# Optimization experiments

Measured on AMD Instinct MI355X. Metric: run time of the kernel, lower is better.

The kernel has to match this reference:

```python
import jax, jax.numpy as jnp
import numpy as np

B, S, IN = 64, 2048, 256          # batch, num_steps, input_size
MS, H, HD = 8, 8, 64              # mem_slots, num_heads, head_size
M = H * HD                        # mem_size = 512
KS = HD                           # key_size defaults to head_size
NG = 2 * M                        # num_gates (gate_style='unit')
TOPK = 3
EPS = 1e-5


def layernorm(x, g, b):
    mu = jnp.mean(x, axis=-1, keepdims=True)
    var = jnp.var(x, axis=-1, keepdims=True)
    return (x - mu) / jnp.sqrt(var + EPS) * g + b


def setup_inputs() -> dict:
    key = jax.random.key(0)
    ks = jax.random.split(key, 16)
    def w(k, shape, scale=0.02):
        return jax.random.normal(k, shape, dtype=jnp.float32) * scale
    return {
        "inputs": jax.random.normal(ks[0], (B, S, IN), dtype=jnp.float32),
        "memory": jax.random.normal(ks[1], (B, MS, M), dtype=jnp.float32),
        "Wq": w(ks[2], (M, H * KS)), "bq": jnp.zeros((H * KS,), jnp.float32),
        "Wk": w(ks[3], (M, H * KS)), "bk": jnp.zeros((H * KS,), jnp.float32),
        "Wv": w(ks[4], (M, H * HD)), "bv": jnp.zeros((H * HD,), jnp.float32),
        "Wmlp": w(ks[5], (M, M)), "bmlp": jnp.zeros((M,), jnp.float32),  # shared across both mlp layers ([Linear]*L)
        "g1": jnp.ones((M,), jnp.float32), "b1": jnp.zeros((M,), jnp.float32),
        "g2": jnp.ones((M,), jnp.float32), "b2": jnp.zeros((M,), jnp.float32),
        "Wi": w(ks[6], (IN, M)), "bi": jnp.zeros((M,), jnp.float32),  # input_projector
        "rw": jax.random.normal(ks[7], (M,), dtype=jnp.float32),       # RepeatLinear.w
        "Wr": w(ks[8], (M, NG)), "br": jnp.zeros((NG,), jnp.float32),  # RepeatLinear.linear
        "Wg": w(ks[9], (MS, M, NG)),                                   # GroupLinearLayer (no bias)
        "forget_bias": jnp.array(1.0, jnp.float32),
        "input_bias": jnp.array(0.0, jnp.float32),
    }


def reference(inputs, memory, Wq, bq, Wk, bk, Wv, bv, Wmlp, bmlp,
              g1, b1, g2, b2, Wi, bi, rw, Wr, br, Wg,
              forget_bias, input_bias):
    # input_projector (treat_input_as_matrix=True path)
    x = inputs @ Wi + bi                                   # [B,S,M]

    # --- multihead attention over memory (num_blocks=1) ---
    q = (memory @ Wq + bq).reshape(B, MS, H, KS).transpose(0, 2, 1, 3)   # [B,H,MS,KS]
    k = (x @ Wk + bk).reshape(B, S, H, KS).transpose(0, 2, 1, 3)         # [B,H,S,KS]
    v = (x @ Wv + bv).reshape(B, S, H, HD).transpose(0, 2, 1, 3)         # [B,H,S,HD]
    scores = jax.nn.softmax(jnp.einsum('bhmd,bhsd->bhms', q, k), axis=-1)  # no 1/sqrt(d) scale, per source
    # top-k mask over key/step axis, scatter of top-k indices -> multiplicative 0/1 mask
    _, idx = jax.lax.top_k(scores, TOPK)                   # [B,H,MS,TOPK]
    mask = jnp.sum(jax.nn.one_hot(idx, S, dtype=scores.dtype), axis=-2)  # [B,H,MS,S]
    scores = scores * mask
    att = jnp.einsum('bhms,bhsd->bhmd', scores, v)         # [B,H,MS,HD]
    att = att.transpose(0, 2, 1, 3).reshape(B, MS, M)      # [B,MS,M]

    mem1 = layernorm(memory + att, g1, b1)
    mlp = jax.nn.relu(mem1 @ Wmlp + bmlp)                  # attention_mlp layer (weights shared)
    mlp = jax.nn.relu(mlp @ Wmlp + bmlp)
    next_mem = layernorm(mem1 + mlp, g2, b2)

    # --- gates (computed from pre-attention memory, per forward_step) ---
    gate_in = jax.nn.relu(rw * x).mean(axis=1) @ Wr + br   # RepeatLinear -> [B,NG]
    gate_mem = jnp.einsum('bsd,sdo->bso', jnp.tanh(memory), Wg)  # GroupLinear -> [B,MS,NG]
    gates = gate_mem + gate_in[:, None, :]
    input_gate, forget_gate = jnp.split(gates, 2, axis=2)  # each [B,MS,M]
    input_gate = jax.nn.sigmoid(input_gate + input_bias)
    forget_gate = jax.nn.sigmoid(forget_gate + forget_bias)

    next_mem = input_gate * jnp.tanh(next_mem) + forget_gate * memory
    return next_mem.reshape(B, MS * M)
```

## Files before the change

### kernel.cpp

```cpp
#include <hip/hip_runtime.h>
#include <hip/hip_bf16.h>
#include <math.h>

#define BB 64
#define SS 2048
#define IN_ 256
#define MSLOT 8
#define HH 8
#define HD_ 64
#define MM 512
#define NG_ 1024

typedef __attribute__((ext_vector_type(8))) short short8;
typedef __attribute__((ext_vector_type(8))) unsigned short ushort8;
typedef __attribute__((ext_vector_type(4))) unsigned short ushort4v;
typedef __attribute__((ext_vector_type(4))) float f32x4;
typedef __attribute__((ext_vector_type(16))) float f32x16;
typedef unsigned long long u64;
typedef unsigned int u32;

__device__ __forceinline__ unsigned short f2bf(float f) {
    unsigned int u = __builtin_bit_cast(unsigned int, f);
    u += 0x7fff + ((u >> 16) & 1);
    return (unsigned short)(u >> 16);
}

__device__ __forceinline__ u32 f2bf_pk(float a, float b) {
    u32 r;
    asm("v_cvt_pk_bf16_f32 %0, %1, %2" : "=v"(r) : "v"(a), "v"(b));
    return r;
}

__device__ __forceinline__ u64 score_key(float v, int idx) {
    u32 x = __float_as_uint(v);
    u32 fk = (x & 0x80000000u) ? ~x : (x | 0x80000000u);
    return ((u64)fk << 32) | (u32)(~(u32)idx);
}
__device__ __forceinline__ float key_val(u64 k) {
    u32 fk = (u32)(k >> 32);
    u32 x = (fk & 0x80000000u) ? (fk & 0x7FFFFFFFu) : ~fk;
    return __uint_as_float(x);
}
__device__ __forceinline__ int key_idx(u64 k) { return (int)(~(u32)k); }

__device__ __forceinline__ void merge3(u64& a0, u64& a1, u64& a2, u64 b0, u64 b1, u64 b2) {
    bool t0 = a0 >= b0;
    u64 m0 = t0 ? a0 : b0;
    u64 a0x = t0 ? a1 : a0, a1x = t0 ? a2 : a1;
    u64 b0x = t0 ? b0 : b1, b1x = t0 ? b1 : b2;
    bool t1 = a0x >= b0x;
    u64 m1 = t1 ? a0x : b0x;
    u64 a0y = t1 ? a1x : a0x;
    u64 b0y = t1 ? b0x : b1x;
    bool t2 = a0y >= b0y;
    u64 m2 = t2 ? a0y : b0y;
    a0 = m0; a1 = m1; a2 = m2;
}

__device__ __forceinline__ void merge3_shfl(u64& k0, u64& k1, u64& k2, int off) {
    u64 b0 = __shfl_xor(k0, off);
    u64 b1 = __shfl_xor(k1, off);
    u64 b2 = __shfl_xor(k2, off);
    merge3(k0, k1, k2, b0, b1, b2);
}

__device__ __forceinline__ float block_sum256(float v, float* red) {
    int t = threadIdx.x;
    red[t] = v; __syncthreads();
    for (int s = 128; s > 0; s >>= 1) {
        if (t < s) red[t] += red[t + s];
        __syncthreads();
    }
    float r = red[0];
    __syncthreads();
    return r;
}

__device__ __forceinline__ void stage_tile_f32cvt(unsigned short* lds,
                                                  const float* __restrict__ src,
                                                  int t) {
#pragma unroll
    for (int it = 0; it < 8; ++it) {
        int c = t + it * 256;
        int r = c >> 5, ch = c & 31;
        const float* p = src + (size_t)r * 256 + ch * 8;
        float4 f0 = *(const float4*)p;
        float4 f1 = *(const float4*)(p + 4);
        uint4 v;
        v.x = f2bf_pk(f0.x, f0.y);
        v.y = f2bf_pk(f0.z, f0.w);
        v.z = f2bf_pk(f1.x, f1.y);
        v.w = f2bf_pk(f1.z, f1.w);
        int sch = ch ^ (r & 15);
        *(uint4*)(lds + r * 256 + sch * 8) = v;
    }
}

__device__ __forceinline__ short8 frag_ld(const unsigned short* lds, int row, int chunk) {
    int sch = chunk ^ (row & 15);
    return *(const short8*)(lds + row * 256 + sch * 8);
}

__device__ __forceinline__ short8 frag_ld512(const unsigned short* lds, int row, int chunk) {
    int sch = chunk ^ (row & 7);
    return *(const short8*)(lds + row * 512 + sch * 8);
}

__global__ __launch_bounds__(256) void k_fuse_w2(const float* __restrict__ Wi,
                                                 const float* __restrict__ Wk,
                                                 const float* __restrict__ Wv,
                                                 const float* __restrict__ bi,
                                                 const float* __restrict__ bv,
                                                 float* __restrict__ WikT,
                                                 float* __restrict__ Wiv,
                                                 float* __restrict__ bvf) {
    int blk = blockIdx.x;
    int t = threadIdx.x;
    if (blk >= 256) {
        int o = (blk - 256) * 256 + t;
        float acc = bv[o];
        for (int j = 0; j < 512; ++j) acc += bi[j] * Wv[j * 512 + o];
        bvf[o] = acc;
        return;
    }
    int which = blk >> 7;
    int rem = blk & 127;
    int ot = rem >> 3, it = rem & 7;
    int o0 = ot * 32, i0 = it * 32;
    const float* W = which ? Wv : Wk;

    __shared__ float As[64 * 33];
    __shared__ float Bs[32 * 65];
    int tx = t & 15, ty = t >> 4;

    float acc[2][2] = {{0.f, 0.f}, {0.f, 0.f}};
    for (int jc = 0; jc < 512; jc += 64) {
        __syncthreads();
#pragma unroll
        for (int k = 0; k < 8; ++k) {
            int idx = t + k * 256;
            int jl = idx >> 5, ol = idx & 31;
            As[jl * 33 + ol] = W[(jc + jl) * 512 + o0 + ol];
        }
#pragma unroll
        for (int k = 0; k < 8; ++k) {
            int idx = t + k * 256;
            int il = idx >> 6, jl = idx & 63;
            Bs[il * 65 + jl] = Wi[(i0 + il) * 512 + jc + jl];
        }
        __syncthreads();
#pragma unroll 4
        for (int jl = 0; jl < 64; ++jl) {
            float a0 = As[jl * 33 + ty], a1 = As[jl * 33 + ty + 16];
            float b0 = Bs[tx * 65 + jl], b1 = Bs[(tx + 16) * 65 + jl];
            acc[0][0] += a0 * b0; acc[0][1] += a0 * b1;
            acc[1][0] += a1 * b0; acc[1][1] += a1 * b1;
        }
    }
#pragma unroll
    for (int m = 0; m < 2; ++m)
#pragma unroll
        for (int n = 0; n < 2; ++n) {
            int o = o0 + ty + 16 * m, i = i0 + tx + 16 * n;
            if (which) Wiv[i * 512 + o] = acc[m][n];
            else       WikT[o * 256 + i] = acc[m][n];
        }
}

__global__ __launch_bounds__(256) void k_q2(const float* __restrict__ memory,
                                            const float* __restrict__ Wq,
                                            const float* __restrict__ bq,
                                            float* __restrict__ q) {
    int blk = blockIdx.x;
    int bt = blk >> 4, ot2 = blk & 15;
    int b0 = bt * 32, o0 = ot2 * 32;
    int t = threadIdx.x;
    __shared__ float Am[32 * 65];
    __shared__ float Bq[64 * 33];
    int tx = t & 15, ty = t >> 4;
    float acc[2][2] = {{0.f, 0.f}, {0.f, 0.f}};
    for (int jc = 0; jc < 512; jc += 64) {
        __syncthreads();
#pragma unroll
        for (int k = 0; k < 8; ++k) {
            int idx = t + k * 256;
            int bl = idx >> 6, jl = idx & 63;
            Am[bl * 65 + jl] = memory[(b0 + bl) * 512 + jc + jl];
        }
#pragma unroll
        for (int k = 0; k < 8; ++k) {
            int idx = t + k * 256;
            int jl = idx >> 5, ol = idx & 31;
            Bq[jl * 33 + ol] = Wq[(jc + jl) * 512 + o0 + ol];
        }
        __syncthreads();
#pragma unroll 4
        for (int jl = 0; jl < 64; ++jl) {
            float a0 = Am[ty * 65 + jl], a1 = Am[(ty + 16) * 65 + jl];
            float b0v = Bq[jl * 33 + tx], b1v = Bq[jl * 33 + tx + 16];
            acc[0][0] += a0 * b0v; acc[0][1] += a0 * b1v;
            acc[1][0] += a1 * b0v; acc[1][1] += a1 * b1v;
        }
    }
#pragma unroll
    for (int m = 0; m < 2; ++m)
#pragma unroll
        for (int n = 0; n < 2; ++n) {
            int bms = b0 + ty + 16 * m, o = o0 + tx + 16 * n;
            q[bms * 512 + o] = acc[m][n] + bq[o];
        }
}

__global__ __launch_bounds__(256) void k_p(const float* __restrict__ q,
                                           const float* __restrict__ WikT,
                                           unsigned short* __restrict__ Pb) {
    int blk = blockIdx.x;
    int b = blk >> 6, hm = blk & 63;
    int h = hm >> 3, ms = hm & 7;
    int t = threadIdx.x;
    __shared__ float qv[64];
    if (t < 64) qv[t] = q[(b * 8 + ms) * 512 + h * 64 + t];
    __syncthreads();
    float acc = 0.f;
    for (int d = 0; d < 64; ++d) acc += qv[d] * WikT[(h * 64 + d) * 256 + t];
    Pb[blk * 256 + t] = f2bf(acc);
}

__global__ __launch_bounds__(256) void k_prep(const float* __restrict__ Wi,
                                              unsigned short* __restrict__ WiTf,
                                              const float* __restrict__ mem,
                                              unsigned short* __restrict__ tm,
                                              const float* __restrict__ Wmlp,
                                              unsigned short* __restrict__ WmlpTb) {
    int blk = blockIdx.x;
    int t = threadIdx.x;
    if (blk < 512) {
        int idx = blk * 256 + t;
        int e = idx & 7, l = (idx >> 3) & 63, ks = (idx >> 9) & 15, dtg = idx >> 13;
        int d = dtg * 32 + (l & 31);
        int k = ks * 16 + (l >> 5) * 8 + e;
        WiTf[idx] = f2bf(Wi[k * 512 + d]);
    } else if (blk < 768) {
        int i = ((blk - 512) * 256 + t) * 4;
        float4 v = *(const float4*)(mem + i);
        ushort4v o;
        o[0] = f2bf(tanhf(v.x)); o[1] = f2bf(tanhf(v.y));
        o[2] = f2bf(tanhf(v.z)); o[3] = f2bf(tanhf(v.w));
        *(ushort4v*)(tm + i) = o;
    } else {
        int o = blk - 768;
#pragma unroll
        for (int kk = 0; kk < 2; ++kk) {
            int k = kk * 256 + t;
            WmlpTb[o * 512 + k] = f2bf(Wmlp[k * 512 + o]);
        }
    }
}

__global__ __launch_bounds__(256) void k_big(const float* __restrict__ inputs,
                                             const unsigned short* __restrict__ Pb,
                                             const unsigned short* __restrict__ WiTf,
                                             const float* __restrict__ bi,
                                             const float* __restrict__ rw,
                                             uint4* __restrict__ statA,
                                             uint4* __restrict__ statB,
                                             float* __restrict__ giaccp) {
    __shared__ unsigned short Il[64 * 256];
    int t = threadIdx.x;
    int hw = blockIdx.x;
    int L = (hw & 7) * 256 + (hw >> 3);
    int b = L >> 5, stile = L & 31;
    int l = t & 63, w = t >> 6;
    int kg = l >> 4, r16 = l & 15;
    int l31 = l & 31, hi = l >> 5;

    short8 a[8];
    {
        const unsigned short* pbase = Pb + ((size_t)(b * 64 + w * 16 + r16)) * 256;
#pragma unroll
        for (int kk = 0; kk < 8; ++kk)
            a[kk] = *(const short8*)(pbase + kk * 32 + kg * 8);
    }

    stage_tile_f32cvt(Il, inputs + ((size_t)b * SS + stile * 64) * IN_, t);
    __syncthreads();

    f32x4 acc[4];
#pragma unroll
    for (int nt = 0; nt < 4; ++nt) acc[nt] = (f32x4){0.f, 0.f, 0.f, 0.f};
#pragma unroll
    for (int kk = 0; kk < 8; ++kk) {
#pragma unroll
        for (int nt = 0; nt < 4; ++nt) {
            short8 bfr = frag_ld(Il, nt * 16 + r16, kk * 4 + kg);
            acc[nt] = __builtin_amdgcn_mfma_f32_16x16x32_bf16(a[kk], bfr, acc[nt], 0, 0, 0);
        }
    }

#pragma unroll 1
    for (int i = 0; i < 4; ++i) {
        int dtg = w * 4 + i;
        int d = dtg * 32 + l31;
        float bid = bi[d], rwd = rw[d];
        f32x16 g0 = {0.f,0.f,0.f,0.f,0.f,0.f,0.f,0.f,0.f,0.f,0.f,0.f,0.f,0.f,0.f,0.f};
        f32x16 g1 = {0.f,0.f,0.f,0.f,0.f,0.f,0.f,0.f,0.f,0.f,0.f,0.f,0.f,0.f,0.f,0.f};
#pragma unroll
        for (int ksh = 0; ksh < 2; ++ksh) {
            short8 wf[8];
#pragma unroll
            for (int ks8 = 0; ks8 < 8; ++ks8)
                wf[ks8] = *(const short8*)(WiTf + ((size_t)((dtg * 16 + ksh * 8 + ks8) * 64) + l) * 8);
#pragma unroll
            for (int ks8 = 0; ks8 < 8; ++ks8) {
                int ch = (ksh * 8 + ks8) * 2 + hi;
                short8 a0 = frag_ld(Il, l31, ch);
                g0 = __builtin_amdgcn_mfma_f32_32x32x16_bf16(a0, wf[ks8], g0, 0, 0, 0);
                short8 a1 = frag_ld(Il, 32 + l31, ch);
                g1 = __builtin_amdgcn_mfma_f32_32x32x16_bf16(a1, wf[ks8], g1, 0, 0, 0);
            }
        }
        float rs = 0.f;
#pragma unroll
        for (int jj = 0; jj < 16; ++jj) {
            rs += fmaxf(rwd * (g0[jj] + bid), 0.f);
            rs += fmaxf(rwd * (g1[jj] + bid), 0.f);
        }
        rs += __shfl_xor(rs, 32);
        if (hi == 0)
            giaccp[((size_t)stile * 64 + b) * 512 + d] = rs;
    }

    __syncthreads();
    float* Sl = (float*)Il;
#pragma unroll
    for (int nt = 0; nt < 4; ++nt)
#pragma unroll
        for (int j = 0; j < 4; ++j)
            Sl[(w * 16 + kg * 4 + j) * 65 + nt * 16 + r16] = acc[nt][j];
    __syncthreads();

    int row = t >> 2, cq = t & 3;
    float v[16];
#pragma unroll
    for (int i = 0; i < 16; ++i) v[i] = Sl[row * 65 + cq * 16 + i];

    u64 k0 = 0, k1 = 0, k2 = 0;
#pragma unroll
    for (int i = 0; i < 16; ++i) {
        u64 key = score_key(v[i], stile * 64 + cq * 16 + i);
        bool g0 = key > k0, g1 = key > k1, g2 = key > k2;
        k2 = g1 ? k1 : (g2 ? key : k2);
        k1 = g0 ? k0 : (g1 ? key : k1);
        k0 = g0 ? key : k0;
    }
    merge3_shfl(k0, k1, k2, 1);
    merge3_shfl(k0, k1, k2, 2);

    float m = key_val(k0);
    float se = 0.f;
#pragma unroll
    for (int i = 0; i < 16; ++i) se += expf(v[i] - m);
    se += __shfl_xor(se, 1);
    se += __shfl_xor(se, 2);

    if (cq == 0) {
        int grow = (b * 64 + row) * 32 + stile;
        statA[grow] = make_uint4(__float_as_uint(se), (u32)(k0 >> 32), (u32)k0, (u32)(k1 >> 32));
        statB[grow] = make_uint4((u32)k1, (u32)(k2 >> 32), (u32)k2, 0u);
    }
}

__global__ __launch_bounds__(256) void k_combine(const uint4* __restrict__ statA,
                                                 const uint4* __restrict__ statB,
                                                 float* __restrict__ topk_p,
                                                 int* __restrict__ topk_idx) {
    int t = threadIdx.x;
    int row = blockIdx.x * 4 + (t >> 6);
    int l = t & 63;

    float s_c = 0.f, m_c = 0.f;
    u64 k0 = 0, k1 = 0, k2 = 0;
    if (l < 32) {
        uint4 A = statA[row * 32 + l];
        uint4 Bv = statB[row * 32 + l];
        s_c = __uint_as_float(A.x);
        k0 = ((u64)A.y << 32) | A.z;
        k1 = ((u64)A.w << 32) | Bv.x;
        k2 = ((u64)Bv.y << 32) | Bv.z;
        m_c = key_val(k0);
    }
    merge3_shfl(k0, k1, k2, 1);
    merge3_shfl(k0, k1, k2, 2);
    merge3_shfl(k0, k1, k2, 4);
    merge3_shfl(k0, k1, k2, 8);
    merge3_shfl(k0, k1, k2, 16);

    float M = key_val(k0);
    float S = (l < 32) ? s_c * expf(m_c - M) : 0.f;
#pragma unroll
    for (int off = 1; off <= 16; off <<= 1) S += __shfl_xor(S, off);

    if (l == 0) {
        u64 ks[3] = {k0, k1, k2};
#pragma unroll
        for (int r = 0; r < 3; ++r) {
            topk_p[row * 3 + r] = expf(key_val(ks[r]) - M) / S;
            topk_idx[row * 3 + r] = key_idx(ks[r]);
        }
    }
}

__global__ __launch_bounds__(256) void k_att2(const float* __restrict__ inputs,
                                              const float* __restrict__ Wiv,
                                              const float* __restrict__ bvf,
                                              const float* __restrict__ topk_p,
                                              const int* __restrict__ topk_idx,
                                              const float* __restrict__ memory,
                                              const float* __restrict__ g1,
                                              const float* __restrict__ b1,
                                              float* __restrict__ mem1) {
    int bms = blockIdx.x;
    int b = bms >> 3, ms = bms & 7;
    int t = threadIdx.x;
    __shared__ float w[8 * 256];
    __shared__ float ps[8];
    __shared__ float red[256];

#pragma unroll
    for (int h = 0; h < 8; ++h) {
        int row = (b * 64 + h * 8 + ms) * 3;
        float acc = 0.f, psum = 0.f;
#pragma unroll
        for (int j = 0; j < 3; ++j) {
            int sj = topk_idx[row + j];
            float pj = topk_p[row + j];
            acc += pj * inputs[((size_t)b * SS + sj) * IN_ + t];
            psum += pj;
        }
        w[h * 256 + t] = acc;
        if (t == 0) ps[h] = psum;
    }
    __syncthreads();

    float a_val[2];
#pragma unroll
    for (int oo = 0; oo < 2; ++oo) {
        int o = oo * 256 + t;
        int h = o >> 6;
        float acc = ps[h] * bvf[o];
        const float* wh = w + h * 256;
#pragma unroll 8
        for (int i = 0; i < 256; ++i) acc += wh[i] * Wiv[i * 512 + o];
        a_val[oo] = acc;
    }

    float m0 = memory[bms * 512 + t], m1 = memory[bms * 512 + t + 256];
    float x0 = m0 + a_val[0], x1 = m1 + a_val[1];
    float mu = block_sum256(x0 + x1, red) * (1.f / 512.f);
    float d0 = x0 - mu, d1 = x1 - mu;
    float var = block_sum256(d0 * d0 + d1 * d1, red) * (1.f / 512.f);
    float rstd = rsqrtf(var + 1e-5f);
    mem1[bms * 512 + t]       = d0 * rstd * g1[t] + b1[t];
    mem1[bms * 512 + t + 256] = d1 * rstd * g1[t + 256] + b1[t + 256];
}

__global__ __launch_bounds__(256) void k_gatein2(const float* __restrict__ giaccp,
                                                 const float* __restrict__ Wr,
                                                 const float* __restrict__ br,
                                                 float* __restrict__ gate_in) {
    int b = blockIdx.x >> 2, ot = blockIdx.x & 3;
    int t = threadIdx.x;
    int o = ot * 256 + t;
    __shared__ float gm[512];
    float s0 = 0.f, s1 = 0.f;
    for (int st = 0; st < 32; ++st) {
        s0 += giaccp[((size_t)st * 64 + b) * 512 + t];
        s1 += giaccp[((size_t)st * 64 + b) * 512 + t + 256];
    }
    gm[t]       = s0 * (1.0f / 2048.0f);
    gm[t + 256] = s1 * (1.0f / 2048.0f);
    __syncthreads();
    float acc = br[o];
#pragma unroll 8
    for (int d = 0; d < 512; ++d) acc += gm[d] * Wr[d * 1024 + o];
    gate_in[b * 1024 + o] = acc;
}

__global__ __launch_bounds__(256) void k_gates_mfma(const unsigned short* __restrict__ tmem_b,
                                                    const float* __restrict__ Wg,
                                                    const float* __restrict__ gate_in,
                                                    const float* __restrict__ fb,
                                                    const float* __restrict__ ib,
                                                    float* __restrict__ sg) {
    int ms = blockIdx.x >> 5;
    int otile = blockIdx.x & 31;
    int t = threadIdx.x;
    int l = t & 63, w = t >> 6;
    int kg = l >> 4, r16 = l & 15;
    __shared__ unsigned short Al[64 * 128];
    __shared__ unsigned short Bl[32 * 136];
    f32x4 acc[2];
#pragma unroll
    for (int nt = 0; nt < 2; ++nt) acc[nt] = (f32x4){0.f, 0.f, 0.f, 0.f};

    int o_l = t & 31;
    for (int kc = 0; kc < 4; ++kc) {
        __syncthreads();
#pragma unroll
        for (int it = 0; it < 4; ++it) {
            int c = t + it * 256;
            int r = c >> 4, ch = c & 15;
            ushort8 v = *(const ushort8*)(tmem_b + (size_t)(r * 8 + ms) * 512 + kc * 128 + ch * 8);
            int sch = ch ^ (r & 7);
            *(ushort8*)(Al + r * 128 + sch * 8) = v;
        }
#pragma unroll
        for (int i = 0; i < 16; ++i) {
            int k_l = (t >> 5) + 8 * i;
            float v = Wg[((size_t)ms * 512 + kc * 128 + k_l) * 1024 + otile * 32 + o_l];
            Bl[o_l * 136 + k_l] = f2bf(v);
        }
        __syncthreads();
#pragma unroll
        for (int kk = 0; kk < 4; ++kk) {
            int ch = kk * 4 + kg;
            short8 a = *(const short8*)(Al + (w * 16 + r16) * 128 + ((ch ^ (r16 & 7)) * 8));
#pragma unroll
            for (int nt = 0; nt < 2; ++nt) {
                short8 bfr = *(const short8*)(Bl + (nt * 16 + r16) * 136 + ch * 8);
                acc[nt] = __builtin_amdgcn_mfma_f32_16x16x32_bf16(a, bfr, acc[nt], 0, 0, 0);
            }
        }
    }
    float ibv = ib[0], fbv = fb[0];
#pragma unroll
    for (int nt = 0; nt < 2; ++nt) {
        int o = otile * 32 + nt * 16 + r16;
        float bias = (o < 512) ? ibv : fbv;
#pragma unroll
        for (int j = 0; j < 4; ++j) {
            int b = w * 16 + kg * 4 + j;
            float g = acc[nt][j] + gate_in[b * 1024 + o] + bias;
            sg[(size_t)(b * 8 + ms) * 1024 + o] = 1.f / (1.f + expf(-g));
        }
    }
}

__global__ __launch_bounds__(256) void k_mlp_mfma(const float* __restrict__ mem1,
                                                  const unsigned short* __restrict__ WmlpTb,
                                                  const float* __restrict__ bmlp,
                                                  const float* __restrict__ g2,
                                                  const float* __restrict__ b2,
                                                  const float* __restrict__ sg,
                                                  const float* __restrict__ memory,
                                                  float* __restrict__ out) {
    __shared__ unsigned short At[16 * 512];
    __shared__ unsigned short Bt[16 * 512];
    __shared__ float redS[64], redQ[64], muL[16], rsL[16];
    int blk = blockIdx.x;
    int rowbase = blk * 16;
    int t = threadIdx.x;
    int l = t & 63, w = t >> 6;
    int kg = l >> 4, r16 = l & 15;

#pragma unroll
    for (int it = 0; it < 4; ++it) {
        int c = t + it * 256;
        int r = c >> 6, ch = c & 63;
        const float* p = mem1 + (size_t)(rowbase + r) * 512 + ch * 8;
        float4 f0 = *(const float4*)p;
        float4 f1 = *(const float4*)(p + 4);
        uint4 v;
        v.x = f2bf_pk(f0.x, f0.y);
        v.y = f2bf_pk(f0.z, f0.w);
        v.z = f2bf_pk(f1.x, f1.y);
        v.w = f2bf_pk(f1.z, f1.w);
        int sch = ch ^ (r & 7);
        *(uint4*)(At + r * 512 + sch * 8) = v;
    }
    __syncthreads();

    f32x4 acc[8];
#pragma unroll
    for (int f = 0; f < 8; ++f) acc[f] = (f32x4){0.f, 0.f, 0.f, 0.f};
    for (int kk2 = 0; kk2 < 16; ++kk2) {
        short8 a = frag_ld512(At, r16, kk2 * 4 + kg);
#pragma unroll
        for (int f = 0; f < 8; ++f) {
            short8 bfr = *(const short8*)(WmlpTb + (size_t)(w * 128 + f * 16 + r16) * 512 + kk2 * 32 + kg * 8);
            acc[f] = __builtin_amdgcn_mfma_f32_16x16x32_bf16(a, bfr, acc[f], 0, 0, 0);
        }
    }
#pragma unroll
    for (int f = 0; f < 8; ++f) {
        int o = w * 128 + f * 16 + r16;
        float bm = bmlp[o];
        int ch = o >> 3, oe = o & 7;
#pragma unroll
        for (int j = 0; j < 4; ++j) {
            int row = kg * 4 + j;
            float v = fmaxf(acc[f][j] + bm, 0.f);
            Bt[row * 512 + ((ch ^ (row & 7)) * 8 + oe)] = f2bf(v);
        }
    }
    __syncthreads();

#pragma unroll
    for (int f = 0; f < 8; ++f) acc[f] = (f32x4){0.f, 0.f, 0.f, 0.f};
    for (int kk2 = 0; kk2 < 16; ++kk2) {
        short8 a = frag_ld512(Bt, r16, kk2 * 4 + kg);
#pragma unroll
        for (int f = 0; f < 8; ++f) {
            short8 bfr = *(const short8*)(WmlpTb + (size_t)(w * 128 + f * 16 + r16) * 512 + kk2 * 32 + kg * 8);
            acc[f] = __builtin_amdgcn_mfma_f32_16x16x32_bf16(a, bfr, acc[f], 0, 0, 0);
        }
    }

    float y[8][4];
    float ps[4] = {0.f, 0.f, 0.f, 0.f}, pq[4] = {0.f, 0.f, 0.f, 0.f};
#pragma unroll
    for (int f = 0; f < 8; ++f) {
        int o = w * 128 + f * 16 + r16;
        float bm = bmlp[o];
#pragma unroll
        for (int j = 0; j < 4; ++j) {
            int row = kg * 4 + j;
            float m1v = mem1[(size_t)(rowbase + row) * 512 + o];
            float v = m1v + fmaxf(acc[f][j] + bm, 0.f);
            y[f][j] = v;
            ps[j] += v;
            pq[j] += v * v;
        }
    }
#pragma unroll
    for (int j = 0; j < 4; ++j) {
#pragma unroll
        for (int off = 1; off <= 8; off <<= 1) {
            ps[j] += __shfl_xor(ps[j], off);
            pq[j] += __shfl_xor(pq[j], off);
        }
    }
    if (r16 == 0) {
#pragma unroll
        for (int j = 0; j < 4; ++j) {
            int row = kg * 4 + j;
            redS[row * 4 + w] = ps[j];
            redQ[row * 4 + w] = pq[j];
        }
    }
    __syncthreads();
    if (t < 16) {
        float s = redS[t * 4] + redS[t * 4 + 1] + redS[t * 4 + 2] + redS[t * 4 + 3];
        float q = redQ[t * 4] + redQ[t * 4 + 1] + redQ[t * 4 + 2] + redQ[t * 4 + 3];
        float mu = s * (1.f / 512.f);
        float var = q * (1.f / 512.f) - mu * mu;
        muL[t] = mu;
        rsL[t] = rsqrtf(var + 1e-5f);
    }
    __syncthreads();

#pragma unroll
    for (int f = 0; f < 8; ++f) {
        int o = w * 128 + f * 16 + r16;
        float g2v = g2[o], b2v = b2[o];
#pragma unroll
        for (int j = 0; j < 4; ++j) {
            int row = kg * 4 + j;
            int grow = rowbase + row;
            float np = (y[f][j] - muL[row]) * rsL[row] * g2v + b2v;
            float ig = sg[(size_t)grow * 1024 + o];
            float fg = sg[(size_t)grow * 1024 + 512 + o];
            float mv = memory[(size_t)grow * 512 + o];
            out[(size_t)grow * 512 + o] = ig * tanhf(np) + fg * mv;
        }
    }
}

extern "C" void kernel_launch(void* const* d_in, const int* in_sizes, int n_in,
                              void* d_out, int out_size, void* d_ws, size_t ws_size,
                              hipStream_t stream) {
    const float* inputs = (const float*)d_in[0];
    const float* memory = (const float*)d_in[1];
    const float* Wq  = (const float*)d_in[2];
    const float* bq  = (const float*)d_in[3];
    const float* Wk  = (const float*)d_in[4];
    const float* Wv  = (const float*)d_in[6];
    const float* bv  = (const float*)d_in[7];
    const float* Wmlp= (const float*)d_in[8];
    const float* bmlp= (const float*)d_in[9];
    const float* g1  = (const float*)d_in[10];
    const float* b1  = (const float*)d_in[11];
    const float* g2  = (const float*)d_in[12];
    const float* b2  = (const float*)d_in[13];
    const float* Wi  = (const float*)d_in[14];
    const float* bi  = (const float*)d_in[15];
    const float* rw  = (const float*)d_in[16];
    const float* Wr  = (const float*)d_in[17];
    const float* br  = (const float*)d_in[18];
    const float* Wg  = (const float*)d_in[19];
    const float* fb  = (const float*)d_in[20];
    const float* ib  = (const float*)d_in[21];
    float* out = (float*)d_out;

    float* ws = (float*)d_ws;
    float* WikT   = ws + 0;
    float* Wiv    = ws + 131072;
    float* bvf    = ws + 262144;
    float* qbuf   = ws + 263168;
    unsigned short* Pb   = (unsigned short*)(ws + 525312);
    unsigned short* WiTf = (unsigned short*)(ws + 1049600);
    uint4* statA  = (uint4*)(ws + 1115136);
    uint4* statB  = (uint4*)(ws + 1639424);
    float* topkp  = ws + 2163712;
    int*   topki  = (int*)(ws + 2176000);
    float* giaccp = ws + 2188288;
    float* gatein = ws + 3236864;
    float* sgbuf  = ws + 3302400;
    float* mem1   = ws + 3826688;
    unsigned short* tmem_b = (unsigned short*)(ws + 4088832);
    unsigned short* WmlpTb = (unsigned short*)(ws + 4219904);

    (void)in_sizes; (void)n_in; (void)out_size; (void)ws_size;

    k_fuse_w2<<<258, 256, 0, stream>>>(Wi, Wk, Wv, bi, bv, WikT, Wiv, bvf);
    k_q2<<<256, 256, 0, stream>>>(memory, Wq, bq, qbuf);
    k_p<<<4096, 256, 0, stream>>>(qbuf, WikT, Pb);
    k_prep<<<1280, 256, 0, stream>>>(Wi, WiTf, memory, tmem_b, Wmlp, WmlpTb);
    k_big<<<2048, 256, 0, stream>>>(inputs, Pb, WiTf, bi, rw, statA, statB, giaccp);
    k_combine<<<1024, 256, 0, stream>>>(statA, statB, topkp, topki);
    k_gatein2<<<256, 256, 0, stream>>>(giaccp, Wr, br, gatein);
    k_gates_mfma<<<256, 256, 0, stream>>>(tmem_b, Wg, gatein, fb, ib, sgbuf);
    k_att2<<<512, 256, 0, stream>>>(inputs, Wiv, bvf, topkp, topki, memory, g1, b1, mem1);
    k_mlp_mfma<<<32, 256, 0, stream>>>(mem1, WmlpTb, bmlp, g2, b2, sgbuf, memory, out);
}
```

Measured before the change: 300.5 us.

## Merge small kernels into fewer launches and restructure k_big MFMA tiling

Folds k_fuse_w2, k_q2 and k_prep into one k_pre launch, merges k_combine with k_gatein2 into k_mid, and merges k_gates_mfma with k_att2 into k_post. This removes launch gaps and tail idling between small dependent kernels. k_big now computes scores with 32x32x16 MFMAs and a separate LDS score buffer, and splits the input-projection work across waves by sequence half and d-group. Partial gate sums double in count (giaccp layout grows), so workspace offsets shift. The extra LDS could lower occupancy in k_big.

```diff
diff --git a/kernel.cpp b/kernel.cpp
--- a/kernel.cpp
+++ b/kernel.cpp
@@ -106,109 +106,131 @@
     return *(const short8*)(lds + row * 512 + sch * 8);
 }
 
-__global__ __launch_bounds__(256) void k_fuse_w2(const float* __restrict__ Wi,
-                                                 const float* __restrict__ Wk,
-                                                 const float* __restrict__ Wv,
-                                                 const float* __restrict__ bi,
-                                                 const float* __restrict__ bv,
-                                                 float* __restrict__ WikT,
-                                                 float* __restrict__ Wiv,
-                                                 float* __restrict__ bvf) {
+__global__ __launch_bounds__(256) void k_pre(const float* __restrict__ Wi,
+                                             const float* __restrict__ Wk,
+                                             const float* __restrict__ Wv,
+                                             const float* __restrict__ bi,
+                                             const float* __restrict__ bv,
+                                             const float* __restrict__ memory,
+                                             const float* __restrict__ Wq,
+                                             const float* __restrict__ bq,
+                                             const float* __restrict__ Wmlp,
+                                             float* __restrict__ WikT,
+                                             float* __restrict__ Wiv,
+                                             float* __restrict__ bvf,
+                                             float* __restrict__ q,
+                                             unsigned short* __restrict__ WiTf,
+                                             unsigned short* __restrict__ tm,
+                                             unsigned short* __restrict__ WmlpTb) {
+    __shared__ float As[64 * 33];
+    __shared__ float Bs[32 * 65];
     int blk = blockIdx.x;
     int t = threadIdx.x;
-    if (blk >= 256) {
+
+    if (blk < 256) {
+        int which = blk >> 7;
+        int rem = blk & 127;
+        int ot = rem >> 3, it = rem & 7;
+        int o0 = ot * 32, i0 = it * 32;
+        const float* W = which ? Wv : Wk;
+        int tx = t & 15, ty = t >> 4;
+        float acc[2][2] = {{0.f, 0.f}, {0.f, 0.f}};
+        for (int jc = 0; jc < 512; jc += 64) {
+            __syncthreads();
+#pragma unroll
+            for (int k = 0; k < 8; ++k) {
+                int idx = t + k * 256;
+                int jl = idx >> 5, ol = idx & 31;
+                As[jl * 33 + ol] = W[(jc + jl) * 512 + o0 + ol];
+            }
+#pragma unroll
+            for (int k = 0; k < 8; ++k) {
+                int idx = t + k * 256;
+                int il = idx >> 6, jl = idx & 63;
+                Bs[il * 65 + jl] = Wi[(i0 + il) * 512 + jc + jl];
+            }
+            __syncthreads();
+#pragma unroll 4
+            for (int jl = 0; jl < 64; ++jl) {
+                float a0 = As[jl * 33 + ty], a1 = As[jl * 33 + ty + 16];
+                float b0 = Bs[tx * 65 + jl], b1 = Bs[(tx + 16) * 65 + jl];
+                acc[0][0] += a0 * b0; acc[0][1] += a0 * b1;
+                acc[1][0] += a1 * b0; acc[1][1] += a1 * b1;
+            }
+        }
+#pragma unroll
+        for (int m = 0; m < 2; ++m)
+#pragma unroll
+            for (int n = 0; n < 2; ++n) {
+                int o = o0 + ty + 16 * m, i = i0 + tx + 16 * n;
+                if (which) Wiv[i * 512 + o] = acc[m][n];
+                else       WikT[o * 256 + i] = acc[m][n];
+            }
+    } else if (blk < 258) {
         int o = (blk - 256) * 256 + t;
         float acc = bv[o];
         for (int j = 0; j < 512; ++j) acc += bi[j] * Wv[j * 512 + o];
         bvf[o] = acc;
-        return;
-    }
-    int which = blk >> 7;
-    int rem = blk & 127;
-    int ot = rem >> 3, it = rem & 7;
-    int o0 = ot * 32, i0 = it * 32;
-    const float* W = which ? Wv : Wk;
-
-    __shared__ float As[64 * 33];
-    __shared__ float Bs[32 * 65];
-    int tx = t & 15, ty = t >> 4;
-
-    float acc[2][2] = {{0.f, 0.f}, {0.f, 0.f}};
-    for (int jc = 0; jc < 512; jc += 64) {
-        __syncthreads();
-#pragma unroll
-        for (int k = 0; k < 8; ++k) {
-            int idx = t + k * 256;
-            int jl = idx >> 5, ol = idx & 31;
-            As[jl * 33 + ol] = W[(jc + jl) * 512 + o0 + ol];
-        }
-#pragma unroll
-        for (int k = 0; k < 8; ++k) {
-            int idx = t + k * 256;
-            int il = idx >> 6, jl = idx & 63;
-            Bs[il * 65 + jl] = Wi[(i0 + il) * 512 + jc + jl];
-        }
-        __syncthreads();
+    } else if (blk < 514) {
+        int qb = blk - 258;
+        int bt = qb >> 4, ot2 = qb & 15;
+        int b0 = bt * 32, o0 = ot2 * 32;
+        int tx = t & 15, ty = t >> 4;
+        float acc[2][2] = {{0.f, 0.f}, {0.f, 0.f}};
+        for (int jc = 0; jc < 512; jc += 64) {
+            __syncthreads();
+#pragma unroll
+            for (int k = 0; k < 8; ++k) {
+                int idx = t + k * 256;
+                int bl = idx >> 6, jl = idx & 63;
+                Bs[bl * 65 + jl] = memory[(b0 + bl) * 512 + jc + jl];
+            }
+#pragma unroll
+            for (int k = 0; k < 8; ++k) {
+                int idx = t + k * 256;
+                int jl = idx >> 5, ol = idx & 31;
+                As[jl * 33 + ol] = Wq[(jc + jl) * 512 + o0 + ol];
+            }
+            __syncthreads();
 #pragma unroll 4
-        for (int jl = 0; jl < 64; ++jl) {
-            float a0 = As[jl * 33 + ty], a1 = As[jl * 33 + ty + 16];
-            float b0 = Bs[tx * 65 + jl], b1 = Bs[(tx + 16) * 65 + jl];
-            acc[0][0] += a0 * b0; acc[0][1] += a0 * b1;
-            acc[1][0] += a1 * b0; acc[1][1] += a1 * b1;
-        }
-    }
-#pragma unroll
-    for (int m = 0; m < 2; ++m)
-#pragma unroll
-        for (int n = 0; n < 2; ++n) {
-            int o = o0 + ty + 16 * m, i = i0 + tx + 16 * n;
-            if (which) Wiv[i * 512 + o] = acc[m][n];
-            else       WikT[o * 256 + i] = acc[m][n];
-        }
-}
-
-__global__ __launch_bounds__(256) void k_q2(const float* __restrict__ memory,
-                                            const float* __restrict__ Wq,
-                                            const float* __restrict__ bq,
-                                            float* __restrict__ q) {
-    int blk = blockIdx.x;
-    int bt = blk >> 4, ot2 = blk & 15;
-    int b0 = bt * 32, o0 = ot2 * 32;
-    int t = threadIdx.x;
-    __shared__ float Am[32 * 65];
-    __shared__ float Bq[64 * 33];
-    int tx = t & 15, ty = t >> 4;
-    float acc[2][2] = {{0.f, 0.f}, {0.f, 0.f}};
-    for (int jc = 0; jc < 512; jc += 64) {
-        __syncthreads();
-#pragma unroll
-        for (int k = 0; k < 8; ++k) {
-            int idx = t + k * 256;
-            int bl = idx >> 6, jl = idx & 63;
-            Am[bl * 65 + jl] = memory[(b0 + bl) * 512 + jc + jl];
-        }
-#pragma unroll
-        for (int k = 0; k < 8; ++k) {
-            int idx = t + k * 256;
-            int jl = idx >> 5, ol = idx & 31;
-            Bq[jl * 33 + ol] = Wq[(jc + jl) * 512 + o0 + ol];
-        }
-        __syncthreads();
-#pragma unroll 4
-        for (int jl = 0; jl < 64; ++jl) {
-            float a0 = Am[ty * 65 + jl], a1 = Am[(ty + 16) * 65 + jl];
-            float b0v = Bq[jl * 33 + tx], b1v = Bq[jl * 33 + tx + 16];
-            acc[0][0] += a0 * b0v; acc[0][1] += a0 * b1v;
-            acc[1][0] += a1 * b0v; acc[1][1] += a1 * b1v;
-        }
-    }
-#pragma unroll
-    for (int m = 0; m < 2; ++m)
-#pragma unroll
-        for (int n = 0; n < 2; ++n) {
-            int bms = b0 + ty + 16 * m, o = o0 + tx + 16 * n;
-            q[bms * 512 + o] = acc[m][n] + bq[o];
-        }
+            for (int jl = 0; jl < 64; ++jl) {
+                float a0 = Bs[ty * 65 + jl], a1 = Bs[(ty + 16) * 65 + jl];
+                float b0v = As[jl * 33 + tx], b1v = As[jl * 33 + tx + 16];
+                acc[0][0] += a0 * b0v; acc[0][1] += a0 * b1v;
+                acc[1][0] += a1 * b0v; acc[1][1] += a1 * b1v;
+            }
+        }
+#pragma unroll
+        for (int m = 0; m < 2; ++m)
+#pragma unroll
+            for (int n = 0; n < 2; ++n) {
+                int bms = b0 + ty + 16 * m, o = o0 + tx + 16 * n;
+                q[bms * 512 + o] = acc[m][n] + bq[o];
+            }
+    } else {
+        int pb = blk - 514;
+        if (pb < 512) {
+            int idx = pb * 256 + t;
+            int e = idx & 7, l = (idx >> 3) & 63, ks = (idx >> 9) & 15, dtg = idx >> 13;
+            int d = dtg * 32 + (l & 31);
+            int k = ks * 16 + (l >> 5) * 8 + e;
+            WiTf[idx] = f2bf(Wi[k * 512 + d]);
+        } else if (pb < 768) {
+            int i = ((pb - 512) * 256 + t) * 4;
+            float4 v = *(const float4*)(memory + i);
+            ushort4v o;
+            o[0] = f2bf(tanhf(v.x)); o[1] = f2bf(tanhf(v.y));
+            o[2] = f2bf(tanhf(v.z)); o[3] = f2bf(tanhf(v.w));
+            *(ushort4v*)(tm + i) = o;
+        } else {
+            int o = pb - 768;
+#pragma unroll
+            for (int kk = 0; kk < 2; ++kk) {
+                int k = kk * 256 + t;
+                WmlpTb[o * 512 + k] = f2bf(Wmlp[k * 512 + o]);
+            }
+        }
+    }
 }
 
 __global__ __launch_bounds__(256) void k_p(const float* __restrict__ q,
@@ -226,37 +248,6 @@
     Pb[blk * 256 + t] = f2bf(acc);
 }
 
-__global__ __launch_bounds__(256) void k_prep(const float* __restrict__ Wi,
-                                              unsigned short* __restrict__ WiTf,
-                                              const float* __restrict__ mem,
-                                              unsigned short* __restrict__ tm,
-                                              const float* __restrict__ Wmlp,
-                                              unsigned short* __restrict__ WmlpTb) {
-    int blk = blockIdx.x;
-    int t = threadIdx.x;
-    if (blk < 512) {
-        int idx = blk * 256 + t;
-        int e = idx & 7, l = (idx >> 3) & 63, ks = (idx >> 9) & 15, dtg = idx >> 13;
-        int d = dtg * 32 + (l & 31);
-        int k = ks * 16 + (l >> 5) * 8 + e;
-        WiTf[idx] = f2bf(Wi[k * 512 + d]);
-    } else if (blk < 768) {
-        int i = ((blk - 512) * 256 + t) * 4;
-        float4 v = *(const float4*)(mem + i);
-        ushort4v o;
-        o[0] = f2bf(tanhf(v.x)); o[1] = f2bf(tanhf(v.y));
-        o[2] = f2bf(tanhf(v.z)); o[3] = f2bf(tanhf(v.w));
-        *(ushort4v*)(tm + i) = o;
-    } else {
-        int o = blk - 768;
-#pragma unroll
-        for (int kk = 0; kk < 2; ++kk) {
-            int k = kk * 256 + t;
-            WmlpTb[o * 512 + k] = f2bf(Wmlp[k * 512 + o]);
-        }
-    }
-}
-
 __global__ __launch_bounds__(256) void k_big(const float* __restrict__ inputs,
                                              const unsigned short* __restrict__ Pb,
                                              const unsigned short* __restrict__ WiTf,
@@ -266,77 +257,64 @@
                                              uint4* __restrict__ statB,
                                              float* __restrict__ giaccp) {
     __shared__ unsigned short Il[64 * 256];
+    __shared__ float Sl[64 * 65];
     int t = threadIdx.x;
     int hw = blockIdx.x;
     int L = (hw & 7) * 256 + (hw >> 3);
     int b = L >> 5, stile = L & 31;
     int l = t & 63, w = t >> 6;
-    int kg = l >> 4, r16 = l & 15;
     int l31 = l & 31, hi = l >> 5;
-
-    short8 a[8];
-    {
-        const unsigned short* pbase = Pb + ((size_t)(b * 64 + w * 16 + r16)) * 256;
-#pragma unroll
-        for (int kk = 0; kk < 8; ++kk)
-            a[kk] = *(const short8*)(pbase + kk * 32 + kg * 8);
-    }
+    int sh = w & 1, dh = w >> 1;
 
     stage_tile_f32cvt(Il, inputs + ((size_t)b * SS + stile * 64) * IN_, t);
     __syncthreads();
 
-    f32x4 acc[4];
-#pragma unroll
-    for (int nt = 0; nt < 4; ++nt) acc[nt] = (f32x4){0.f, 0.f, 0.f, 0.f};
-#pragma unroll
-    for (int kk = 0; kk < 8; ++kk) {
-#pragma unroll
-        for (int nt = 0; nt < 4; ++nt) {
-            short8 bfr = frag_ld(Il, nt * 16 + r16, kk * 4 + kg);
-            acc[nt] = __builtin_amdgcn_mfma_f32_16x16x32_bf16(a[kk], bfr, acc[nt], 0, 0, 0);
+    {
+        f32x16 sacc = {0.f,0.f,0.f,0.f,0.f,0.f,0.f,0.f,0.f,0.f,0.f,0.f,0.f,0.f,0.f,0.f};
+        const unsigned short* pbase = Pb + ((size_t)(b * 64 + dh * 32 + l31)) * 256;
+#pragma unroll
+        for (int ks = 0; ks < 16; ++ks) {
+            short8 pf = *(const short8*)(pbase + ks * 16 + hi * 8);
+            short8 ilf = frag_ld(Il, sh * 32 + l31, ks * 2 + hi);
+            sacc = __builtin_amdgcn_mfma_f32_32x32x16_bf16(pf, ilf, sacc, 0, 0, 0);
+        }
+#pragma unroll
+        for (int r = 0; r < 16; ++r) {
+            int hm = dh * 32 + (r & 3) + 8 * (r >> 2) + 4 * hi;
+            Sl[hm * 65 + sh * 32 + l31] = sacc[r];
         }
     }
 
 #pragma unroll 1
-    for (int i = 0; i < 4; ++i) {
-        int dtg = w * 4 + i;
-        int d = dtg * 32 + l31;
-        float bid = bi[d], rwd = rw[d];
+    for (int grp = 0; grp < 4; ++grp) {
+        int dtg0 = dh * 8 + grp * 2, dtg1 = dtg0 + 1;
         f32x16 g0 = {0.f,0.f,0.f,0.f,0.f,0.f,0.f,0.f,0.f,0.f,0.f,0.f,0.f,0.f,0.f,0.f};
         f32x16 g1 = {0.f,0.f,0.f,0.f,0.f,0.f,0.f,0.f,0.f,0.f,0.f,0.f,0.f,0.f,0.f,0.f};
 #pragma unroll
-        for (int ksh = 0; ksh < 2; ++ksh) {
-            short8 wf[8];
-#pragma unroll
-            for (int ks8 = 0; ks8 < 8; ++ks8)
-                wf[ks8] = *(const short8*)(WiTf + ((size_t)((dtg * 16 + ksh * 8 + ks8) * 64) + l) * 8);
-#pragma unroll
-            for (int ks8 = 0; ks8 < 8; ++ks8) {
-                int ch = (ksh * 8 + ks8) * 2 + hi;
-                short8 a0 = frag_ld(Il, l31, ch);
-                g0 = __builtin_amdgcn_mfma_f32_32x32x16_bf16(a0, wf[ks8], g0, 0, 0, 0);
-                short8 a1 = frag_ld(Il, 32 + l31, ch);
-                g1 = __builtin_amdgcn_mfma_f32_32x32x16_bf16(a1, wf[ks8], g1, 0, 0, 0);
-            }
-        }
-        float rs = 0.f;
-#pragma unroll
-        for (int jj = 0; jj < 16; ++jj) {
-            rs += fmaxf(rwd * (g0[jj] + bid), 0.f);
-            rs += fmaxf(rwd * (g1[jj] + bid), 0.f);
-        }
-        rs += __shfl_xor(rs, 32);
-        if (hi == 0)
-            giaccp[((size_t)stile * 64 + b) * 512 + d] = rs;
-    }
-
-    __syncthreads();
-    float* Sl = (float*)Il;
-#pragma unroll
-    for (int nt = 0; nt < 4; ++nt)
-#pragma unroll
-        for (int j = 0; j < 4; ++j)
-            Sl[(w * 16 + kg * 4 + j) * 65 + nt * 16 + r16] = acc[nt][j];
+        for (int ks = 0; ks < 16; ++ks) {
+            short8 ilf = frag_ld(Il, sh * 32 + l31, ks * 2 + hi);
+            short8 wf0 = *(const short8*)(WiTf + ((size_t)(dtg0 * 16 + ks) * 64 + l) * 8);
+            short8 wf1 = *(const short8*)(WiTf + ((size_t)(dtg1 * 16 + ks) * 64 + l) * 8);
+            g0 = __builtin_amdgcn_mfma_f32_32x32x16_bf16(ilf, wf0, g0, 0, 0, 0);
+            g1 = __builtin_amdgcn_mfma_f32_32x32x16_bf16(ilf, wf1, g1, 0, 0, 0);
+        }
+        int d0 = dtg0 * 32 + l31, d1 = dtg1 * 32 + l31;
+        float bid0 = bi[d0], rwd0 = rw[d0];
+        float bid1 = bi[d1], rwd1 = rw[d1];
+        float rs0 = 0.f, rs1 = 0.f;
+#pragma unroll
+        for (int r = 0; r < 16; ++r) {
+            rs0 += fmaxf(rwd0 * (g0[r] + bid0), 0.f);
+            rs1 += fmaxf(rwd1 * (g1[r] + bid1), 0.f);
+        }
+        rs0 += __shfl_xor(rs0, 32);
+        rs1 += __shfl_xor(rs1, 32);
+        if (hi == 0) {
+            size_t base = ((size_t)(stile * 2 + sh) * 64 + b) * 512;
+            giaccp[base + d0] = rs0;
+            giaccp[base + d1] = rs1;
+        }
+    }
     __syncthreads();
 
     int row = t >> 2, cq = t & 3;
@@ -370,47 +348,76 @@
     }
 }
 
-__global__ __launch_bounds__(256) void k_combine(const uint4* __restrict__ statA,
-                                                 const uint4* __restrict__ statB,
-                                                 float* __restrict__ topk_p,
-                                                 int* __restrict__ topk_idx) {
+__global__ __launch_bounds__(256) void k_mid(const uint4* __restrict__ statA,
+                                             const uint4* __restrict__ statB,
+                                             const float* __restrict__ giaccp,
+                                             const float* __restrict__ Wr,
+                                             const float* __restrict__ br,
+                                             float* __restrict__ topk_p,
+                                             int* __restrict__ topk_idx,
+                                             float* __restrict__ gate_in) {
+    __shared__ float gm[512];
+    int blk = blockIdx.x;
     int t = threadIdx.x;
-    int row = blockIdx.x * 4 + (t >> 6);
-    int l = t & 63;
-
-    float s_c = 0.f, m_c = 0.f;
-    u64 k0 = 0, k1 = 0, k2 = 0;
-    if (l < 32) {
-        uint4 A = statA[row * 32 + l];
-        uint4 Bv = statB[row * 32 + l];
-        s_c = __uint_as_float(A.x);
-        k0 = ((u64)A.y << 32) | A.z;
-        k1 = ((u64)A.w << 32) | Bv.x;
-        k2 = ((u64)Bv.y << 32) | Bv.z;
-        m_c = key_val(k0);
-    }
-    merge3_shfl(k0, k1, k2, 1);
-    merge3_shfl(k0, k1, k2, 2);
-    merge3_shfl(k0, k1, k2, 4);
-    merge3_shfl(k0, k1, k2, 8);
-    merge3_shfl(k0, k1, k2, 16);
-
-    float M = key_val(k0);
-    float S = (l < 32) ? s_c * expf(m_c - M) : 0.f;
-#pragma unroll
-    for (int off = 1; off <= 16; off <<= 1) S += __shfl_xor(S, off);
-
-    if (l == 0) {
-        u64 ks[3] = {k0, k1, k2};
-#pragma unroll
-        for (int r = 0; r < 3; ++r) {
-            topk_p[row * 3 + r] = expf(key_val(ks[r]) - M) / S;
-            topk_idx[row * 3 + r] = key_idx(ks[r]);
-        }
-    }
-}
-
-__global__ __launch_bounds__(256) void k_att2(const float* __restrict__ inputs,
+    if (blk < 1024) {
+        int row = blk * 4 + (t >> 6);
+        int l = t & 63;
+        float s_c = 0.f, m_c = 0.f;
+        u64 k0 = 0, k1 = 0, k2 = 0;
+        if (l < 32) {
+            uint4 A = statA[row * 32 + l];
+            uint4 Bv = statB[row * 32 + l];
+            s_c = __uint_as_float(A.x);
+            k0 = ((u64)A.y << 32) | A.z;
+            k1 = ((u64)A.w << 32) | Bv.x;
+            k2 = ((u64)Bv.y << 32) | Bv.z;
+            m_c = key_val(k0);
+        }
+        merge3_shfl(k0, k1, k2, 1);
+        merge3_shfl(k0, k1, k2, 2);
+        merge3_shfl(k0, k1, k2, 4);
+        merge3_shfl(k0, k1, k2, 8);
+        merge3_shfl(k0, k1, k2, 16);
+
+        float M = key_val(k0);
+        float S = (l < 32) ? s_c * expf(m_c - M) : 0.f;
+#pragma unroll
+        for (int off = 1; off <= 16; off <<= 1) S += __shfl_xor(S, off);
+
+        if (l == 0) {
+            u64 ks[3] = {k0, k1, k2};
+#pragma unroll
+            for (int r = 0; r < 3; ++r) {
+                topk_p[row * 3 + r] = expf(key_val(ks[r]) - M) / S;
+                topk_idx[row * 3 + r] = key_idx(ks[r]);
+            }
+        }
+    } else {
+        int gb = blk - 1024;
+        int b = gb >> 2, ot = gb & 3;
+        int o = ot * 256 + t;
+        float s0 = 0.f, s1 = 0.f;
+        for (int st = 0; st < 64; ++st) {
+            s0 += giaccp[((size_t)st * 64 + b) * 512 + t];
+            s1 += giaccp[((size_t)st * 64 + b) * 512 + t + 256];
+        }
+        gm[t]       = s0 * (1.0f / 2048.0f);
+        gm[t + 256] = s1 * (1.0f / 2048.0f);
+        __syncthreads();
+        float acc = br[o];
+#pragma unroll 8
+        for (int d = 0; d < 512; ++d) acc += gm[d] * Wr[d * 1024 + o];
+        gate_in[b * 1024 + o] = acc;
+    }
+}
+
+__global__ __launch_bounds__(256) void k_post(const unsigned short* __restrict__ tmem_b,
+                                              const float* __restrict__ Wg,
+                                              const float* __restrict__ gate_in,
+                                              const float* __restrict__ fb,
+                                              const float* __restrict__ ib,
+                                              float* __restrict__ sg,
+                                              const float* __restrict__ inputs,
                                               const float* __restrict__ Wiv,
                                               const float* __restrict__ bvf,
                                               const float* __restrict__ topk_p,
@@ -419,130 +426,104 @@
                                               const float* __restrict__ g1,
                                               const float* __restrict__ b1,
                                               float* __restrict__ mem1) {
-    int bms = blockIdx.x;
-    int b = bms >> 3, ms = bms & 7;
+    __shared__ __align__(16) char smem[25088];
+    int blk = blockIdx.x;
     int t = threadIdx.x;
-    __shared__ float w[8 * 256];
-    __shared__ float ps[8];
-    __shared__ float red[256];
-
-#pragma unroll
-    for (int h = 0; h < 8; ++h) {
-        int row = (b * 64 + h * 8 + ms) * 3;
-        float acc = 0.f, psum = 0.f;
-#pragma unroll
-        for (int j = 0; j < 3; ++j) {
-            int sj = topk_idx[row + j];
-            float pj = topk_p[row + j];
-            acc += pj * inputs[((size_t)b * SS + sj) * IN_ + t];
-            psum += pj;
-        }
-        w[h * 256 + t] = acc;
-        if (t == 0) ps[h] = psum;
-    }
-    __syncthreads();
-
-    float a_val[2];
-#pragma unroll
-    for (int oo = 0; oo < 2; ++oo) {
-        int o = oo * 256 + t;
-        int h = o >> 6;
-        float acc = ps[h] * bvf[o];
-        const float* wh = w + h * 256;
+    if (blk < 256) {
+        unsigned short* Al = (unsigned short*)smem;
+        unsigned short* Bl = (unsigned short*)(smem + 16384);
+        int ms = blk >> 5;
+        int otile = blk & 31;
+        int l = t & 63, w = t >> 6;
+        int kg = l >> 4, r16 = l & 15;
+        f32x4 acc[2];
+#pragma unroll
+        for (int nt = 0; nt < 2; ++nt) acc[nt] = (f32x4){0.f, 0.f, 0.f, 0.f};
+
+        int o_l = t & 31;
+        for (int kc = 0; kc < 4; ++kc) {
+            __syncthreads();
+#pragma unroll
+            for (int it = 0; it < 4; ++it) {
+                int c = t + it * 256;
+                int r = c >> 4, ch = c & 15;
+                ushort8 v = *(const ushort8*)(tmem_b + (size_t)(r * 8 + ms) * 512 + kc * 128 + ch * 8);
+                int sch = ch ^ (r & 7);
+                *(ushort8*)(Al + r * 128 + sch * 8) = v;
+            }
+#pragma unroll
+            for (int i = 0; i < 16; ++i) {
+                int k_l = (t >> 5) + 8 * i;
+                float v = Wg[((size_t)ms * 512 + kc * 128 + k_l) * 1024 + otile * 32 + o_l];
+                Bl[o_l * 136 + k_l] = f2bf(v);
+            }
+            __syncthreads();
+#pragma unroll
+            for (int kk = 0; kk < 4; ++kk) {
+                int ch = kk * 4 + kg;
+                short8 a = *(const short8*)(Al + (w * 16 + r16) * 128 + ((ch ^ (r16 & 7)) * 8));
+#pragma unroll
+                for (int nt = 0; nt < 2; ++nt) {
+                    short8 bfr = *(const short8*)(Bl + (nt * 16 + r16) * 136 + ch * 8);
+                    acc[nt] = __builtin_amdgcn_mfma_f32_16x16x32_bf16(a, bfr, acc[nt], 0, 0, 0);
+                }
+            }
+        }
+        float ibv = ib[0], fbv = fb[0];
+#pragma unroll
+        for (int nt = 0; nt < 2; ++nt) {
+            int o = otile * 32 + nt * 16 + r16;
+            float bias = (o < 512) ? ibv : fbv;
+#pragma unroll
+            for (int j = 0; j < 4; ++j) {
+                int b = w * 16 + kg * 4 + j;
+                float g = acc[nt][j] + gate_in[b * 1024 + o] + bias;
+                sg[(size_t)(b * 8 + ms) * 1024 + o] = 1.f / (1.f + expf(-g));
+            }
+        }
+    } else {
+        float* wbuf = (float*)smem;
+        float* ps   = (float*)(smem + 8192);
+        float* red  = (float*)(smem + 8224);
+        int bms = blk - 256;
+        int b = bms >> 3, ms = bms & 7;
+
+#pragma unroll
+        for (int h = 0; h < 8; ++h) {
+            int row = (b * 64 + h * 8 + ms) * 3;
+            float acc = 0.f, psum = 0.f;
+#pragma unroll
+            for (int j = 0; j < 3; ++j) {
+                int sj = topk_idx[row + j];
+                float pj = topk_p[row + j];
+                acc += pj * inputs[((size_t)b * SS + sj) * IN_ + t];
+                psum += pj;
+            }
+            wbuf[h * 256 + t] = acc;
+            if (t == 0) ps[h] = psum;
+        }
+        __syncthreads();
+
+        float a_val[2];
+#pragma unroll
+        for (int oo = 0; oo < 2; ++oo) {
+            int o = oo * 256 + t;
+            int h = o >> 6;
+            float acc = ps[h] * bvf[o];
+            const float* wh = wbuf + h * 256;
 #pragma unroll 8
-        for (int i = 0; i < 256; ++i) acc += wh[i] * Wiv[i * 512 + o];
-        a_val[oo] = acc;
-    }
-
-    float m0 = memory[bms * 512 + t], m1 = memory[bms * 512 + t + 256];
-    float x0 = m0 + a_val[0], x1 = m1 + a_val[1];
-    float mu = block_sum256(x0 + x1, red) * (1.f / 512.f);
-    float d0 = x0 - mu, d1 = x1 - mu;
-    float var = block_sum256(d0 * d0 + d1 * d1, red) * (1.f / 512.f);
-    float rstd = rsqrtf(var + 1e-5f);
-    mem1[bms * 512 + t]       = d0 * rstd * g1[t] + b1[t];
-    mem1[bms * 512 + t + 256] = d1 * rstd * g1[t + 256] + b1[t + 256];
-}
-
-__global__ __launch_bounds__(256) void k_gatein2(const float* __restrict__ giaccp,
-                                                 const float* __restrict__ Wr,
-                                                 const float* __restrict__ br,
-                                                 float* __restrict__ gate_in) {
-    int b = blockIdx.x >> 2, ot = blockIdx.x & 3;
-    int t = threadIdx.x;
-    int o = ot * 256 + t;
-    __shared__ float gm[512];
-    float s0 = 0.f, s1 = 0.f;
-    for (int st = 0; st < 32; ++st) {
-        s0 += giaccp[((size_t)st * 64 + b) * 512 + t];
-        s1 += giaccp[((size_t)st * 64 + b) * 512 + t + 256];
-    }
-    gm[t]       = s0 * (1.0f / 2048.0f);
-    gm[t + 256] = s1 * (1.0f / 2048.0f);
-    __syncthreads();
-    float acc = br[o];
-#pragma unroll 8
-    for (int d = 0; d < 512; ++d) acc += gm[d] * Wr[d * 1024 + o];
-    gate_in[b * 1024 + o] = acc;
-}
-
-__global__ __launch_bounds__(256) void k_gates_mfma(const unsigned short* __restrict__ tmem_b,
-                                                    const float* __restrict__ Wg,
-                                                    const float* __restrict__ gate_in,
-                                                    const float* __restrict__ fb,
-                                                    const float* __restrict__ ib,
-                                                    float* __restrict__ sg) {
-    int ms = blockIdx.x >> 5;
-    int otile = blockIdx.x & 31;
-    int t = threadIdx.x;
-    int l = t & 63, w = t >> 6;
-    int kg = l >> 4, r16 = l & 15;
-    __shared__ unsigned short Al[64 * 128];
-    __shared__ unsigned short Bl[32 * 136];
-    f32x4 acc[2];
-#pragma unroll
-    for (int nt = 0; nt < 2; ++nt) acc[nt] = (f32x4){0.f, 0.f, 0.f, 0.f};
-
-    int o_l = t & 31;
-    for (int kc = 0; kc < 4; ++kc) {
-        __syncthreads();
-#pragma unroll
-        for (int it = 0; it < 4; ++it) {
-            int c = t + it * 256;
-            int r = c >> 4, ch = c & 15;
-            ushort8 v = *(const ushort8*)(tmem_b + (size_t)(r * 8 + ms) * 512 + kc * 128 + ch * 8);
-            int sch = ch ^ (r & 7);
-            *(ushort8*)(Al + r * 128 + sch * 8) = v;
-        }
-#pragma unroll
-        for (int i = 0; i < 16; ++i) {
-            int k_l = (t >> 5) + 8 * i;
-            float v = Wg[((size_t)ms * 512 + kc * 128 + k_l) * 1024 + otile * 32 + o_l];
-            Bl[o_l * 136 + k_l] = f2bf(v);
-        }
-        __syncthreads();
-#pragma unroll
-        for (int kk = 0; kk < 4; ++kk) {
-            int ch = kk * 4 + kg;
-            short8 a = *(const short8*)(Al + (w * 16 + r16) * 128 + ((ch ^ (r16 & 7)) * 8));
-#pragma unroll
-            for (int nt = 0; nt < 2; ++nt) {
-                short8 bfr = *(const short8*)(Bl + (nt * 16 + r16) * 136 + ch * 8);
-                acc[nt] = __builtin_amdgcn_mfma_f32_16x16x32_bf16(a, bfr, acc[nt], 0, 0, 0);
-            }
-        }
-    }
-    float ibv = ib[0], fbv = fb[0];
-#pragma unroll
-    for (int nt = 0; nt < 2; ++nt) {
-        int o = otile * 32 + nt * 16 + r16;
-        float bias = (o < 512) ? ibv : fbv;
-#pragma unroll
-        for (int j = 0; j < 4; ++j) {
-            int b = w * 16 + kg * 4 + j;
-            float g = acc[nt][j] + gate_in[b * 1024 + o] + bias;
-            sg[(size_t)(b * 8 + ms) * 1024 + o] = 1.f / (1.f + expf(-g));
-        }
+            for (int i = 0; i < 256; ++i) acc += wh[i] * Wiv[i * 512 + o];
+            a_val[oo] = acc;
+        }
+
+        float m0 = memory[bms * 512 + t], m1 = memory[bms * 512 + t + 256];
+        float x0 = m0 + a_val[0], x1 = m1 + a_val[1];
+        float mu = block_sum256(x0 + x1, red) * (1.f / 512.f);
+        float d0 = x0 - mu, d1 = x1 - mu;
+        float var = block_sum256(d0 * d0 + d1 * d1, red) * (1.f / 512.f);
+        float rstd = rsqrtf(var + 1e-5f);
+        mem1[bms * 512 + t]       = d0 * rstd * g1[t] + b1[t];
+        mem1[bms * 512 + t + 256] = d1 * rstd * g1[t + 256] + b1[t + 256];
     }
 }
 
@@ -714,22 +695,20 @@
     float* topkp  = ws + 2163712;
     int*   topki  = (int*)(ws + 2176000);
     float* giaccp = ws + 2188288;
-    float* gatein = ws + 3236864;
-    float* sgbuf  = ws + 3302400;
-    float* mem1   = ws + 3826688;
-    unsigned short* tmem_b = (unsigned short*)(ws + 4088832);
-    unsigned short* WmlpTb = (unsigned short*)(ws + 4219904);
+    float* gatein = ws + 4285440;
+    float* sgbuf  = ws + 4350976;
+    float* mem1   = ws + 4875264;
+    unsigned short* tmem_b = (unsigned short*)(ws + 5137408);
+    unsigned short* WmlpTb = (unsigned short*)(ws + 5268480);
 
     (void)in_sizes; (void)n_in; (void)out_size; (void)ws_size;
 
-    k_fuse_w2<<<258, 256, 0, stream>>>(Wi, Wk, Wv, bi, bv, WikT, Wiv, bvf);
-    k_q2<<<256, 256, 0, stream>>>(memory, Wq, bq, qbuf);
+    k_pre<<<1794, 256, 0, stream>>>(Wi, Wk, Wv, bi, bv, memory, Wq, bq, Wmlp,
+                                    WikT, Wiv, bvf, qbuf, WiTf, tmem_b, WmlpTb);
     k_p<<<4096, 256, 0, stream>>>(qbuf, WikT, Pb);
-    k_prep<<<1280, 256, 0, stream>>>(Wi, WiTf, memory, tmem_b, Wmlp, WmlpTb);
     k_big<<<2048, 256, 0, stream>>>(inputs, Pb, WiTf, bi, rw, statA, statB, giaccp);
-    k_combine<<<1024, 256, 0, stream>>>(statA, statB, topkp, topki);
-    k_gatein2<<<256, 256, 0, stream>>>(giaccp, Wr, br, gatein);
-    k_gates_mfma<<<256, 256, 0, stream>>>(tmem_b, Wg, gatein, fb, ib, sgbuf);
-    k_att2<<<512, 256, 0, stream>>>(inputs, Wiv, bvf, topkp, topki, memory, g1, b1, mem1);
+    k_mid<<<1280, 256, 0, stream>>>(statA, statB, giaccp, Wr, br, topkp, topki, gatein);
+    k_post<<<768, 256, 0, stream>>>(tmem_b, Wg, gatein, fb, ib, sgbuf,
+                                    inputs, Wiv, bvf, topkp, topki, memory, g1, b1, mem1);
     k_mlp_mfma<<<32, 256, 0, stream>>>(mem1, WmlpTb, bmlp, g2, b2, sgbuf, memory, out);
 }
```

After: 256.8 us. 14.5% less time.
